# Optimization experiments

Hardware: AMD Instinct MI355X
Metric: run time of the kernel (lower is better)

Reference implementation:

```python
import jax, jax.numpy as jnp
import numpy as np

N = 100000   # nodes per branch
E = 1600000  # edges per branch
B = 512      # graphs in batch
D = 256      # input feature dim
C = 27       # number of side-effect labels
NEG_SLOPE = 0.2


def _gat_conv(x, src, dst, W, a_src, a_dst, b):
    """PyG GATConv, heads=1, with self loops. x:[N,din], src/dst:[E+N]."""
    n = x.shape[0]
    h = x @ W                               # [N, dout]
    al_s = h @ a_src                        # [N]
    al_d = h @ a_dst                        # [N]
    e = jax.nn.leaky_relu(al_s[src] + al_d[dst], NEG_SLOPE)  # [E+N]
    # segment softmax over destination nodes (self loops guarantee non-empty)
    m = jax.ops.segment_max(e, dst, num_segments=n)
    w = jnp.exp(e - m[dst])
    denom = jax.ops.segment_sum(w, dst, num_segments=n)
    alpha = w / denom[dst]                  # [E+N]
    out = jax.ops.segment_sum(h[src] * alpha[:, None], dst, num_segments=n)
    return out + b


def _with_self_loops(edge_index, n):
    loop = jnp.arange(n, dtype=edge_index.dtype)
    src = jnp.concatenate([edge_index[0], loop])
    dst = jnp.concatenate([edge_index[1], loop])
    return src, dst


def _mean_pool(x, batch, num_graphs):
    s = jax.ops.segment_sum(x, batch, num_segments=num_graphs)
    cnt = jax.ops.segment_sum(jnp.ones(x.shape[0], x.dtype), batch, num_segments=num_graphs)
    return s / jnp.maximum(cnt, 1.0)[:, None]


def _gat_params(key, din, dout):
    k = jax.random.split(key, 4)
    sc = 1.0 / np.sqrt(din)
    return (jax.random.normal(k[0], (din, dout), jnp.float32) * sc,
            jax.random.normal(k[1], (dout,), jnp.float32) * sc,
            jax.random.normal(k[2], (dout,), jnp.float32) * sc,
            jnp.zeros((dout,), jnp.float32))


def setup_inputs() -> dict:
    key = jax.random.key(0)
    ks = jax.random.split(key, 12)
    inp = {
        'x_s': jax.random.normal(ks[0], (N, D), jnp.float32),
        'x_t': jax.random.normal(ks[1], (N, D), jnp.float32),
        'edge_index_s': jax.random.randint(ks[2], (2, E), 0, N, jnp.int32),
        'edge_index_t': jax.random.randint(ks[3], (2, E), 0, N, jnp.int32),
        'xs_batch': jnp.sort(jax.random.randint(ks[4], (N,), 0, B, jnp.int32)),
        'xt_batch': jnp.sort(jax.random.randint(ks[5], (N,), 0, B, jnp.int32)),
    }
    for name, kk, din, dout in [('s1', ks[6], D, D // 2), ('s2', ks[7], D // 2, D // 4),
                                 ('t1', ks[8], D, D // 2), ('t2', ks[9], D // 2, D // 4)]:
        W, a_s, a_d, b = _gat_params(kk, din, dout)
        inp[f'W_{name}'] = W
        inp[f'a_src_{name}'] = a_s
        inp[f'a_dst_{name}'] = a_d
        inp[f'b_{name}'] = b
    inp['lin_w'] = jax.random.normal(ks[10], (D // 4, C), jnp.float32) / np.sqrt(D // 4)
    inp['lin_b'] = jnp.zeros((C,), jnp.float32)
    return inp


def reference(x_s, x_t,
              W_s1, a_src_s1, a_dst_s1, b_s1,
              W_s2, a_src_s2, a_dst_s2, b_s2,
              W_t1, a_src_t1, a_dst_t1, b_t1,
              W_t2, a_src_t2, a_dst_t2, b_t2,
              lin_w, lin_b,
              edge_index_s, edge_index_t, xs_batch, xt_batch):
    src_s, dst_s = _with_self_loops(edge_index_s, N)
    src_t, dst_t = _with_self_loops(edge_index_t, N)

    x1 = _gat_conv(x_s, src_s, dst_s, W_s1, a_src_s1, a_dst_s1, b_s1)
    x2 = _gat_conv(x1, src_s, dst_s, W_s2, a_src_s2, a_dst_s2, b_s2)
    xs = _mean_pool(x2, xs_batch, B)

    x3 = _gat_conv(x_t, src_t, dst_t, W_t1, a_src_t1, a_dst_t1, b_t1)
    x4 = _gat_conv(x3, src_t, dst_t, W_t2, a_src_t2, a_dst_t2, b_t2)
    xt = _mean_pool(x4, xt_batch, B)

    out = (xs + xt) @ lin_w + lin_b        # [B, C]
    return jax.nn.sigmoid(out)
```

## Files before the change

kernel.cpp:

```cpp
#include <hip/hip_runtime.h>
#include <hip/hip_bf16.h>
#include <math.h>

#define NEG_SLOPE 0.2f

static const int NN = 100000;
static const int EE = 1600000;
static const int BB = 512;
static const int NTOT = 2 * NN;
static const int ETOT = 2 * EE;
static const int NBUK = (NTOT + 511) / 512;
static const int CHUNK = 4096;
static const int NBLK = (ETOT + CHUNK - 1) / CHUNK;
static const int GB = (NN + 63) / 64;

typedef __attribute__((ext_vector_type(8))) short bf16x8;
typedef __attribute__((ext_vector_type(4))) float f32x4;

__device__ __forceinline__ float leaky(float x) { return x >= 0.f ? x : NEG_SLOPE * x; }

__device__ __forceinline__ unsigned short f2b(float f) {
    __hip_bfloat16 h = __float2bfloat16(f);
    return *reinterpret_cast<unsigned short*>(&h);
}
__device__ __forceinline__ float b2f_lo(unsigned v) { return __uint_as_float(v << 16); }
__device__ __forceinline__ float b2f_hi(unsigned v) { return __uint_as_float(v & 0xFFFF0000u); }
__device__ __forceinline__ unsigned packb(float a, float b) {
    return (unsigned)f2b(a) | ((unsigned)f2b(b) << 16);
}

__global__ void wt2_kernel(const float* __restrict__ Ws, const float* __restrict__ Wt_,
                           unsigned short* __restrict__ WT, int K, int N) {
    int idx = blockIdx.x * blockDim.x + threadIdx.x;
    if (idx >= 2 * K * N) return;
    int br = idx >= K * N;
    int j = idx - br * K * N;
    int n = j / K, k = j - n * K;
    const float* W = br ? Wt_ : Ws;
    WT[idx] = f2b(W[(size_t)k * N + n]);
}

template <int K, int N, bool ABF>
__global__ __launch_bounds__(256, 3) void gemm_fused_kernel(
        const void* __restrict__ Av_s, const void* __restrict__ Av_t,
        const unsigned short* __restrict__ WT,
        const float* __restrict__ as_s, const float* __restrict__ ad_s,
        const float* __restrict__ as_t, const float* __restrict__ ad_t,
        unsigned* __restrict__ hb, float* __restrict__ al_s, float* __restrict__ al_d,
        int nblk) {
    constexpr int NT2 = N / 32;
    __shared__ float als0[64], ald0[64];
    const int bid = blockIdx.x;
    const int br = (bid >= nblk) ? 1 : 0;
    const int lb = bid - br * nblk;
    const int t = threadIdx.x;
    const int l = t & 63, w = t >> 6;
    const int wm = w >> 1, wn = w & 1;
    const int rl = l & 15, kh = l >> 4;
    const int row0 = lb * 64 + wm * 32;
    const int r0 = min(row0 + rl, NN - 1);
    const int r1 = min(row0 + 16 + rl, NN - 1);
    const void* Av = br ? Av_t : Av_s;
    const unsigned short* WTb = WT + (size_t)br * N * K;
    const float* asv = br ? as_t : as_s;
    const float* adv = br ? ad_t : ad_s;

    f32x4 acc[2][NT2];
    #pragma unroll
    for (int g = 0; g < 2; g++)
        #pragma unroll
        for (int q = 0; q < NT2; q++) acc[g][q] = (f32x4){0.f, 0.f, 0.f, 0.f};

    if constexpr (ABF) {
        const unsigned short* A = (const unsigned short*)Av;
        bf16x8 A0[4], A1[4];
        #pragma unroll
        for (int kb = 0; kb < 4; kb++) {
            A0[kb] = *(const bf16x8*)(A + (size_t)r0 * K + kb * 32 + kh * 8);
            A1[kb] = *(const bf16x8*)(A + (size_t)r1 * K + kb * 32 + kh * 8);
        }
        #pragma unroll
        for (int kb = 0; kb < 4; kb++) {
            #pragma unroll
            for (int q = 0; q < NT2; q++) {
                int c = wn * (N / 2) + q * 16 + rl;
                bf16x8 bv = *(const bf16x8*)(WTb + (size_t)c * K + kb * 32 + kh * 8);
                acc[0][q] = __builtin_amdgcn_mfma_f32_16x16x32_bf16(A0[kb], bv, acc[0][q], 0, 0, 0);
                acc[1][q] = __builtin_amdgcn_mfma_f32_16x16x32_bf16(A1[kb], bv, acc[1][q], 0, 0, 0);
            }
        }
    } else {
        const float* A = (const float*)Av;
        #pragma unroll
        for (int kc = 0; kc < K; kc += 128) {
            float4 A0[8], A1[8];
            #pragma unroll
            for (int kb = 0; kb < 4; kb++) {
                const float* p0 = A + (size_t)r0 * K + kc + kb * 32 + kh * 8;
                const float* p1 = A + (size_t)r1 * K + kc + kb * 32 + kh * 8;
                A0[2 * kb] = *(const float4*)p0;
                A0[2 * kb + 1] = *(const float4*)(p0 + 4);
                A1[2 * kb] = *(const float4*)p1;
                A1[2 * kb + 1] = *(const float4*)(p1 + 4);
            }
            #pragma unroll
            for (int kb = 0; kb < 4; kb++) {
                float4 x0 = A0[2 * kb], x1 = A0[2 * kb + 1];
                float4 y0 = A1[2 * kb], y1 = A1[2 * kb + 1];
                union { bf16x8 v; unsigned short u[8]; } au, bu;
                au.u[0] = f2b(x0.x); au.u[1] = f2b(x0.y); au.u[2] = f2b(x0.z); au.u[3] = f2b(x0.w);
                au.u[4] = f2b(x1.x); au.u[5] = f2b(x1.y); au.u[6] = f2b(x1.z); au.u[7] = f2b(x1.w);
                bu.u[0] = f2b(y0.x); bu.u[1] = f2b(y0.y); bu.u[2] = f2b(y0.z); bu.u[3] = f2b(y0.w);
                bu.u[4] = f2b(y1.x); bu.u[5] = f2b(y1.y); bu.u[6] = f2b(y1.z); bu.u[7] = f2b(y1.w);
                #pragma unroll
                for (int q = 0; q < NT2; q++) {
                    int c = wn * (N / 2) + q * 16 + rl;
                    bf16x8 bv = *(const bf16x8*)(WTb + (size_t)c * K + kc + kb * 32 + kh * 8);
                    acc[0][q] = __builtin_amdgcn_mfma_f32_16x16x32_bf16(au.v, bv, acc[0][q], 0, 0, 0);
                    acc[1][q] = __builtin_amdgcn_mfma_f32_16x16x32_bf16(bu.v, bv, acc[1][q], 0, 0, 0);
                }
            }
        }
    }

    float asr[NT2], adr[NT2];
    #pragma unroll
    for (int q = 0; q < NT2; q++) {
        int c = wn * (N / 2) + q * 16 + rl;
        asr[q] = asv[c];
        adr[q] = adv[c];
    }

    float psA[2][4], pdA[2][4];
    #pragma unroll
    for (int rg = 0; rg < 2; rg++) {
        #pragma unroll
        for (int i = 0; i < 4; i++) {
            float ps = 0.f, pd = 0.f;
            #pragma unroll
            for (int q = 0; q < NT2; q++) {
                float v = acc[rg][q][i];
                ps += v * asr[q];
                pd += v * adr[q];
            }
            #pragma unroll
            for (int off = 1; off < 16; off <<= 1) {
                ps += __shfl_xor(ps, off);
                pd += __shfl_xor(pd, off);
            }
            psA[rg][i] = ps;
            pdA[rg][i] = pd;
        }
    }
    if (wn == 0 && rl == 0) {
        #pragma unroll
        for (int rg = 0; rg < 2; rg++)
            #pragma unroll
            for (int i = 0; i < 4; i++) {
                int rloc = wm * 32 + rg * 16 + kh * 4 + i;
                als0[rloc] = psA[rg][i];
                ald0[rloc] = pdA[rg][i];
            }
    }
    __syncthreads();
    if (wn == 1 && rl == 0) {
        #pragma unroll
        for (int rg = 0; rg < 2; rg++)
            #pragma unroll
            for (int i = 0; i < 4; i++) {
                int rloc = wm * 32 + rg * 16 + kh * 4 + i;
                int rlocal = lb * 64 + rloc;
                if (rlocal < NN) {
                    int g = br * NN + rlocal;
                    al_s[g] = psA[rg][i] + als0[rloc];
                    al_d[g] = pdA[rg][i] + ald0[rloc];
                }
            }
    }
    #pragma unroll
    for (int rg = 0; rg < 2; rg++) {
        #pragma unroll
        for (int i = 0; i < 4; i++) {
            int rlocal = lb * 64 + wm * 32 + rg * 16 + kh * 4 + i;
            bool ok = (rlocal < NN);
            int g = br * NN + rlocal;
            #pragma unroll
            for (int q = 0; q < NT2; q++) {
                float v = acc[rg][q][i];
                float hi = __shfl_xor(v, 1);
                if (ok && !(rl & 1)) {
                    int c = wn * (N / 2) + q * 16 + rl;
                    hb[(size_t)g * (N / 2) + (c >> 1)] = packb(v, hi);
                }
            }
        }
    }
}

__global__ __launch_bounds__(256) void bin_sort_kernel(const int* __restrict__ src_s,
                                                       const int* __restrict__ dst_s,
                                                       const int* __restrict__ src_t,
                                                       const int* __restrict__ dst_t,
                                                       uint2* __restrict__ region,
                                                       int* __restrict__ shist) {
    __shared__ int hist[512];
    __shared__ int part[256];
    __shared__ int cur[512];
    __shared__ uint2 lbuf[CHUNK];
    const int b = blockIdx.x, t = threadIdx.x;
    const int base = b * CHUNK;
    const int cnt = min(CHUNK, ETOT - base);
    hist[t] = 0; hist[t + 256] = 0;
    __syncthreads();
    unsigned es[16], ed[16];
    #pragma unroll
    for (int i = 0; i < 16; i++) {
        int li = i * 256 + t;
        if (li < cnt) {
            int e = base + li;
            if (e < EE) {
                es[i] = (unsigned)src_s[e];
                ed[i] = (unsigned)dst_s[e];
            } else {
                es[i] = (unsigned)src_t[e - EE] + NN;
                ed[i] = (unsigned)dst_t[e - EE] + NN;
            }
            atomicAdd(&hist[ed[i] >> 9], 1);
        }
    }
    __syncthreads();
    int d0 = hist[2 * t], d1 = hist[2 * t + 1];
    int s = d0 + d1;
    part[t] = s;
    __syncthreads();
    for (int off = 1; off < 256; off <<= 1) {
        int u = (t >= off) ? part[t - off] : 0;
        __syncthreads();
        part[t] += u;
        __syncthreads();
    }
    int ex = part[t] - s;
    cur[2 * t] = ex;
    cur[2 * t + 1] = ex + d0;
    if (2 * t < NBUK + 1) shist[(2 * t) * NBLK + b] = ex;
    if (2 * t + 1 < NBUK + 1) shist[(2 * t + 1) * NBLK + b] = ex + d0;
    __syncthreads();
    #pragma unroll
    for (int i = 0; i < 16; i++) {
        int li = i * 256 + t;
        if (li < cnt) {
            int slot = atomicAdd(&cur[ed[i] >> 9], 1);
            lbuf[slot] = make_uint2(es[i], ed[i]);
        }
    }
    __syncthreads();
    for (int i = t; i < cnt; i += 256) region[base + i] = lbuf[i];
}

__global__ void bucket_tot_kernel(const int* __restrict__ shist, int* __restrict__ btot) {
    __shared__ int red[256];
    const int k = blockIdx.x, t = threadIdx.x;
    int s = 0;
    for (int b = t; b < NBLK; b += 256)
        s += shist[(k + 1) * NBLK + b] - shist[k * NBLK + b];
    red[t] = s;
    __syncthreads();
    for (int off = 128; off > 0; off >>= 1) {
        if (t < off) red[t] += red[t + off];
        __syncthreads();
    }
    if (t == 0) btot[k] = red[0];
}

__global__ void bucket_scan_kernel(const int* __restrict__ btot, int* __restrict__ bbase) {
    __shared__ int part[256];
    int t = threadIdx.x;
    int v0 = (2 * t < NBUK) ? btot[2 * t] : 0;
    int v1 = (2 * t + 1 < NBUK) ? btot[2 * t + 1] : 0;
    int s = v0 + v1;
    part[t] = s;
    __syncthreads();
    for (int off = 1; off < 256; off <<= 1) {
        int u = (t >= off) ? part[t - off] : 0;
        __syncthreads();
        part[t] += u;
        __syncthreads();
    }
    int ex = part[t] - s;
    if (2 * t < NBUK) bbase[2 * t] = ex;
    if (2 * t + 1 < NBUK) bbase[2 * t + 1] = ex + v0;
}

__global__ __launch_bounds__(256) void csr_bucket_kernel(const uint2* __restrict__ region,
                                                         const int* __restrict__ shist,
                                                         const int* __restrict__ bbase,
                                                         int* __restrict__ rowptr,
                                                         int* __restrict__ col) {
    __shared__ int deg[512];
    __shared__ int part[256];
    __shared__ int cur[512];
    const int k = blockIdx.x, t = threadIdx.x;
    const int n0 = k * 512;
    const int nloc = min(512, NTOT - n0);
    const int base = bbase[k];
    deg[t] = 0; deg[t + 256] = 0;
    __syncthreads();
    for (int b = t; b < NBLK; b += 256) {
        int s0 = shist[k * NBLK + b], s1 = shist[(k + 1) * NBLK + b];
        for (int i = s0; i < s1; i++) {
            uint2 e = region[(size_t)b * CHUNK + i];
            atomicAdd(&deg[(int)e.y - n0], 1);
        }
    }
    __syncthreads();
    int d0 = deg[2 * t], d1 = deg[2 * t + 1];
    int s = d0 + d1;
    part[t] = s;
    __syncthreads();
    for (int off = 1; off < 256; off <<= 1) {
        int u = (t >= off) ? part[t - off] : 0;
        __syncthreads();
        part[t] += u;
        __syncthreads();
    }
    int ex = part[t] - s;
    cur[2 * t] = ex;
    cur[2 * t + 1] = ex + d0;
    if (2 * t < nloc) rowptr[n0 + 2 * t] = base + ex;
    if (2 * t + 1 < nloc) rowptr[n0 + 2 * t + 1] = base + ex + d0;
    if (t == 0 && n0 + nloc == NTOT) rowptr[NTOT] = base + part[255];
    __syncthreads();
    for (int b = t; b < NBLK; b += 256) {
        int s0 = shist[k * NBLK + b], s1 = shist[(k + 1) * NBLK + b];
        for (int i = s0; i < s1; i++) {
            uint2 e = region[(size_t)b * CHUNK + i];
            int pos = atomicAdd(&cur[(int)e.y - n0], 1);
            col[base + pos] = (int)e.x;
        }
    }
}

__global__ void brow2_kernel(const int* __restrict__ bs, const int* __restrict__ bt,
                             int* __restrict__ brow_s, int* __restrict__ brow_t) {
    int g = blockIdx.x * blockDim.x + threadIdx.x;
    const int* batch;
    int* brow;
    int gg;
    if (g <= BB) { batch = bs; brow = brow_s; gg = g; }
    else if (g <= 2 * BB + 1) { batch = bt; brow = brow_t; gg = g - (BB + 1); }
    else return;
    int lo = 0, hi = NN;
    while (lo < hi) {
        int mid = (lo + hi) >> 1;
        if (batch[mid] < gg) lo = mid + 1; else hi = mid;
    }
    brow[gg] = lo;
}

__global__ void gat_gather128_kernel(const int* __restrict__ rowptr, const int* __restrict__ col,
                                     const float* __restrict__ al_s, const float* __restrict__ al_d,
                                     const unsigned* __restrict__ hb,
                                     const float* __restrict__ bias_s,
                                     const float* __restrict__ bias_t,
                                     unsigned* __restrict__ outb) {
    int node = blockIdx.x * 4 + (threadIdx.x >> 6);
    int lane = threadIdx.x & 63;
    if (node >= NTOT) return;
    const float* bias = (node < NN) ? bias_s : bias_t;
    const int slot = lane >> 4, sub = lane & 15;
    const int beg = rowptr[node], end = rowptr[node + 1];
    const float ald = al_d[node];
    const float e_self = leaky(al_s[node] + ald);

    float acc[8] = {};
    float dsum = 0.f;
    for (int base = beg; base < end; base += 64) {
        int i = base + lane;
        float w = 0.f; int s = 0;
        if (i < end) {
            s = col[i];
            w = expf(leaky(al_s[s] + ald));
        }
        dsum += w;
        int cnt = min(64, end - base);
        for (int j = 0; j < cnt; j += 4) {
            int idx = j + slot;
            float wj = __shfl(w, idx);
            int sj = __shfl(s, idx);
            uint4 v = *(const uint4*)(hb + (size_t)sj * 64 + sub * 4);
            acc[0] += wj * b2f_lo(v.x); acc[1] += wj * b2f_hi(v.x);
            acc[2] += wj * b2f_lo(v.y); acc[3] += wj * b2f_hi(v.y);
            acc[4] += wj * b2f_lo(v.z); acc[5] += wj * b2f_hi(v.z);
            acc[6] += wj * b2f_lo(v.w); acc[7] += wj * b2f_hi(v.w);
        }
    }
    #pragma unroll
    for (int k = 0; k < 8; k++) {
        acc[k] += __shfl_xor(acc[k], 16);
        acc[k] += __shfl_xor(acc[k], 32);
    }
    #pragma unroll
    for (int off = 32; off > 0; off >>= 1) dsum += __shfl_xor(dsum, off);

    float wself = expf(e_self);
    dsum += wself;
    float inv = 1.f / dsum;
    if (slot == 0) {
        uint4 sv = *(const uint4*)(hb + (size_t)node * 64 + sub * 4);
        float sf[8] = { b2f_lo(sv.x), b2f_hi(sv.x), b2f_lo(sv.y), b2f_hi(sv.y),
                        b2f_lo(sv.z), b2f_hi(sv.z), b2f_lo(sv.w), b2f_hi(sv.w) };
        float o[8];
        #pragma unroll
        for (int k = 0; k < 8; k++)
            o[k] = bias[sub * 8 + k] + (acc[k] + wself * sf[k]) * inv;
        uint4 r = make_uint4(packb(o[0], o[1]), packb(o[2], o[3]),
                             packb(o[4], o[5]), packb(o[6], o[7]));
        *(uint4*)(outb + (size_t)node * 64 + sub * 4) = r;
    }
}

__global__ void gat_gather64_kernel(const int* __restrict__ rowptr, const int* __restrict__ col,
                                    const float* __restrict__ al_s, const float* __restrict__ al_d,
                                    const unsigned* __restrict__ hb,
                                    const float* __restrict__ bias_s,
                                    const float* __restrict__ bias_t,
                                    float* __restrict__ out) {
    int node = blockIdx.x * 4 + (threadIdx.x >> 6);
    int lane = threadIdx.x & 63;
    if (node >= NTOT) return;
    const float* bias = (node < NN) ? bias_s : bias_t;
    const int slot = lane >> 4, sub = lane & 15;
    const int beg = rowptr[node], end = rowptr[node + 1];
    const float ald = al_d[node];
    const float e_self = leaky(al_s[node] + ald);

    float acc[4] = {};
    float dsum = 0.f;
    for (int base = beg; base < end; base += 64) {
        int i = base + lane;
        float w = 0.f; int s = 0;
        if (i < end) {
            s = col[i];
            w = expf(leaky(al_s[s] + ald));
        }
        dsum += w;
        int cnt = min(64, end - base);
        for (int j = 0; j < cnt; j += 4) {
            int idx = j + slot;
            float wj = __shfl(w, idx);
            int sj = __shfl(s, idx);
            uint2 v = *(const uint2*)(hb + (size_t)sj * 32 + sub * 2);
            acc[0] += wj * b2f_lo(v.x); acc[1] += wj * b2f_hi(v.x);
            acc[2] += wj * b2f_lo(v.y); acc[3] += wj * b2f_hi(v.y);
        }
    }
    #pragma unroll
    for (int k = 0; k < 4; k++) {
        acc[k] += __shfl_xor(acc[k], 16);
        acc[k] += __shfl_xor(acc[k], 32);
    }
    #pragma unroll
    for (int off = 32; off > 0; off >>= 1) dsum += __shfl_xor(dsum, off);

    float wself = expf(e_self);
    dsum += wself;
    float inv = 1.f / dsum;
    if (slot == 0) {
        uint2 sv = *(const uint2*)(hb + (size_t)node * 32 + sub * 2);
        float sf[4] = { b2f_lo(sv.x), b2f_hi(sv.x), b2f_lo(sv.y), b2f_hi(sv.y) };
        float4 o;
        o.x = bias[sub * 4 + 0] + (acc[0] + wself * sf[0]) * inv;
        o.y = bias[sub * 4 + 1] + (acc[1] + wself * sf[1]) * inv;
        o.z = bias[sub * 4 + 2] + (acc[2] + wself * sf[2]) * inv;
        o.w = bias[sub * 4 + 3] + (acc[3] + wself * sf[3]) * inv;
        *(float4*)(out + (size_t)node * 64 + sub * 4) = o;
    }
}

__global__ void pool_seg_kernel(const float* __restrict__ x,
                                const int* __restrict__ brow_s, const int* __restrict__ brow_t,
                                float* __restrict__ pooled_s, float* __restrict__ pooled_t) {
    __shared__ float red[4][64];
    int g = blockIdx.x;
    int tb = g >= BB;
    int gb = g - tb * BB;
    const int* brow = tb ? brow_t : brow_s;
    float* pooled = tb ? pooled_t : pooled_s;
    int off = tb ? NN : 0;
    int lane = threadIdx.x & 63, w = threadIdx.x >> 6;
    int beg = brow[gb], end = brow[gb + 1];
    float acc = 0.f;
    for (int n = beg + w; n < end; n += 4)
        acc += x[(size_t)(off + n) * 64 + lane];
    red[w][lane] = acc;
    __syncthreads();
    if (w == 0) {
        float s = red[0][lane] + red[1][lane] + red[2][lane] + red[3][lane];
        float cnt = (float)(end - beg);
        pooled[(size_t)gb * 64 + lane] = s / fmaxf(cnt, 1.f);
    }
}

__global__ void final_kernel(const float* __restrict__ ps, const float* __restrict__ pt,
                             const float* __restrict__ lw, const float* __restrict__ lb,
                             float* __restrict__ out) {
    int g = blockIdx.x;
    int c = threadIdx.x;
    if (c >= 27) return;
    float acc = lb[c];
    #pragma unroll 8
    for (int k = 0; k < 64; k++) {
        float xv = ps[g * 64 + k] + pt[g * 64 + k];
        acc += xv * lw[k * 27 + c];
    }
    out[g * 27 + c] = 1.f / (1.f + expf(-acc));
}

extern "C" void kernel_launch(void* const* d_in, const int* in_sizes, int n_in,
                              void* d_out, int out_size, void* d_ws, size_t ws_size,
                              hipStream_t stream) {
    const float* x_s = (const float*)d_in[0];
    const float* x_t = (const float*)d_in[1];
    const int* ei_s = (const int*)d_in[2];
    const int* ei_t = (const int*)d_in[3];
    const int* xs_batch = (const int*)d_in[4];
    const int* xt_batch = (const int*)d_in[5];
    const float* W_s1 = (const float*)d_in[6];
    const float* a_src_s1 = (const float*)d_in[7];
    const float* a_dst_s1 = (const float*)d_in[8];
    const float* b_s1 = (const float*)d_in[9];
    const float* W_s2 = (const float*)d_in[10];
    const float* a_src_s2 = (const float*)d_in[11];
    const float* a_dst_s2 = (const float*)d_in[12];
    const float* b_s2 = (const float*)d_in[13];
    const float* W_t1 = (const float*)d_in[14];
    const float* a_src_t1 = (const float*)d_in[15];
    const float* a_dst_t1 = (const float*)d_in[16];
    const float* b_t1 = (const float*)d_in[17];
    const float* W_t2 = (const float*)d_in[18];
    const float* a_src_t2 = (const float*)d_in[19];
    const float* a_dst_t2 = (const float*)d_in[20];
    const float* b_t2 = (const float*)d_in[21];
    const float* lin_w = (const float*)d_in[22];
    const float* lin_b = (const float*)d_in[23];
    float* out = (float*)d_out;

    unsigned* hb = (unsigned*)d_ws;
    uint2* region = (uint2*)d_ws;
    unsigned* out1b = hb + (size_t)NTOT * 64;
    float* out2 = (float*)out1b;
    int* col = (int*)(out1b + (size_t)NTOT * 64);
    float* al_s = (float*)(col + ETOT);
    float* al_d = al_s + NTOT;
    float* pooled_s = al_d + NTOT;
    float* pooled_t = pooled_s + (size_t)BB * 64;
    unsigned short* WT1 = (unsigned short*)(pooled_t + (size_t)BB * 64);
    unsigned short* WT2 = WT1 + 2 * 256 * 128;
    int* rowptr = (int*)(WT2 + 2 * 128 * 64);
    int* shist = rowptr + NTOT + 1;
    int* btot = shist + (NBUK + 1) * NBLK;
    int* bbase = btot + NBUK;
    int* brow_s = bbase + NBUK;
    int* brow_t = brow_s + BB + 1;

    const int* src_s = ei_s;
    const int* dst_s = ei_s + EE;
    const int* src_t = ei_t;
    const int* dst_t = ei_t + EE;

    bin_sort_kernel<<<NBLK, 256, 0, stream>>>(src_s, dst_s, src_t, dst_t, region, shist);
    bucket_tot_kernel<<<NBUK, 256, 0, stream>>>(shist, btot);
    bucket_scan_kernel<<<1, 256, 0, stream>>>(btot, bbase);
    csr_bucket_kernel<<<NBUK, 256, 0, stream>>>(region, shist, bbase, rowptr, col);

    wt2_kernel<<<(2 * 256 * 128 + 255) / 256, 256, 0, stream>>>(W_s1, W_t1, WT1, 256, 128);
    gemm_fused_kernel<256, 128, false><<<2 * GB, 256, 0, stream>>>(
        x_s, x_t, WT1, a_src_s1, a_dst_s1, a_src_t1, a_dst_t1, hb, al_s, al_d, GB);
    gat_gather128_kernel<<<(NTOT + 3) / 4, 256, 0, stream>>>(
        rowptr, col, al_s, al_d, hb, b_s1, b_t1, out1b);

    wt2_kernel<<<(2 * 128 * 64 + 255) / 256, 256, 0, stream>>>(W_s2, W_t2, WT2, 128, 64);
    gemm_fused_kernel<128, 64, true><<<2 * GB, 256, 0, stream>>>(
        out1b, (const unsigned short*)out1b + (size_t)NN * 128, WT2,
        a_src_s2, a_dst_s2, a_src_t2, a_dst_t2, hb, al_s, al_d, GB);
    gat_gather64_kernel<<<(NTOT + 3) / 4, 256, 0, stream>>>(
        rowptr, col, al_s, al_d, hb, b_s2, b_t2, out2);

    brow2_kernel<<<(2 * (BB + 1) + 255) / 256, 256, 0, stream>>>(xs_batch, xt_batch, brow_s, brow_t);
    pool_seg_kernel<<<2 * BB, 256, 0, stream>>>(out2, brow_s, brow_t, pooled_s, pooled_t);
    final_kernel<<<BB, 32, 0, stream>>>(pooled_s, pooled_t, lin_w, lin_b, out);
}
```

Measured before the change: 518.1 us.

## Stage GEMM A tiles through LDS with swizzle; unroll edge gather loops by two

The fused GEMM now copies each 64-row A tile in two K-halves from global memory into shared memory using direct global-to-LDS loads with an XOR swizzle, then reads MFMA operands from LDS. Previously each lane loaded scattered row fragments straight from global memory. This is meant to make the A loads coalesced and to prefetch B fragments per half. Separately, both aggregation kernels now process two neighbors per iteration so more gathers are in flight. The edge loop can read past cnt within the 64-lane chunk, but those lanes carry w=0 and s=0, so it is still safe. The costs are extra LDS use and two barriers per half, which may reduce occupancy.

```diff
diff --git a/kernel.cpp b/kernel.cpp
--- a/kernel.cpp
+++ b/kernel.cpp
@@ -29,6 +29,12 @@
     return (unsigned)f2b(a) | ((unsigned)f2b(b) << 16);
 }
 
+__device__ __forceinline__ void gload_lds16(const void* g, void* l) {
+    __builtin_amdgcn_global_load_lds(
+        (const __attribute__((address_space(1))) void*)g,
+        (__attribute__((address_space(3))) void*)l, 16, 0, 0);
+}
+
 __global__ void wt2_kernel(const float* __restrict__ Ws, const float* __restrict__ Wt_,
                            unsigned short* __restrict__ WT, int K, int N) {
     int idx = blockIdx.x * blockDim.x + threadIdx.x;
@@ -49,7 +55,17 @@
         unsigned* __restrict__ hb, float* __restrict__ al_s, float* __restrict__ al_d,
         int nblk) {
     constexpr int NT2 = N / 32;
+    constexpr int ES = ABF ? 2 : 4;
+    constexpr int ROWB = (K / 2) * ES;
+    constexpr int CPR = ROWB / 16;
+    constexpr int STB = 64 * ROWB;
+    constexpr int IPW = (STB / 16) / 256;
+    constexpr int SWZ = (CPR - 1) < 15 ? (CPR - 1) : 15;
+    constexpr int KBH = (K / 2) / 32;
+
+    __shared__ __align__(16) unsigned char Atile[STB];
     __shared__ float als0[64], ald0[64];
+
     const int bid = blockIdx.x;
     const int br = (bid >= nblk) ? 1 : 0;
     const int lb = bid - br * nblk;
@@ -57,10 +73,8 @@
     const int l = t & 63, w = t >> 6;
     const int wm = w >> 1, wn = w & 1;
     const int rl = l & 15, kh = l >> 4;
-    const int row0 = lb * 64 + wm * 32;
-    const int r0 = min(row0 + rl, NN - 1);
-    const int r1 = min(row0 + 16 + rl, NN - 1);
-    const void* Av = br ? Av_t : Av_s;
+    const int row0blk = lb * 64;
+    const char* Ab = (const char*)(br ? Av_t : Av_s);
     const unsigned short* WTb = WT + (size_t)br * N * K;
     const float* asv = br ? as_t : as_s;
     const float* adv = br ? ad_t : ad_s;
@@ -71,56 +85,58 @@
         #pragma unroll
         for (int q = 0; q < NT2; q++) acc[g][q] = (f32x4){0.f, 0.f, 0.f, 0.f};
 
-    if constexpr (ABF) {
-        const unsigned short* A = (const unsigned short*)Av;
-        bf16x8 A0[4], A1[4];
-        #pragma unroll
-        for (int kb = 0; kb < 4; kb++) {
-            A0[kb] = *(const bf16x8*)(A + (size_t)r0 * K + kb * 32 + kh * 8);
-            A1[kb] = *(const bf16x8*)(A + (size_t)r1 * K + kb * 32 + kh * 8);
-        }
-        #pragma unroll
-        for (int kb = 0; kb < 4; kb++) {
+    #pragma unroll
+    for (int h = 0; h < 2; h++) {
+        #pragma unroll
+        for (int i = 0; i < IPW; i++) {
+            int c = (i * 4 + w) * 64 + l;
+            int row = c / CPR, jp = c % CPR;
+            int jg = jp ^ (row & SWZ);
+            int rowg = min(row0blk + row, NN - 1);
+            const char* src = Ab + ((size_t)rowg * K + h * (K / 2)) * ES + jg * 16;
+            gload_lds16(src, Atile + c * 16);
+        }
+        bf16x8 Bv[KBH * NT2];
+        #pragma unroll
+        for (int kb = 0; kb < KBH; kb++)
             #pragma unroll
             for (int q = 0; q < NT2; q++) {
                 int c = wn * (N / 2) + q * 16 + rl;
-                bf16x8 bv = *(const bf16x8*)(WTb + (size_t)c * K + kb * 32 + kh * 8);
-                acc[0][q] = __builtin_amdgcn_mfma_f32_16x16x32_bf16(A0[kb], bv, acc[0][q], 0, 0, 0);
-                acc[1][q] = __builtin_amdgcn_mfma_f32_16x16x32_bf16(A1[kb], bv, acc[1][q], 0, 0, 0);
-            }
-        }
-    } else {
-        const float* A = (const float*)Av;
-        #pragma unroll
-        for (int kc = 0; kc < K; kc += 128) {
-            float4 A0[8], A1[8];
-            #pragma unroll
-            for (int kb = 0; kb < 4; kb++) {
-                const float* p0 = A + (size_t)r0 * K + kc + kb * 32 + kh * 8;
-                const float* p1 = A + (size_t)r1 * K + kc + kb * 32 + kh * 8;
-                A0[2 * kb] = *(const float4*)p0;
-                A0[2 * kb + 1] = *(const float4*)(p0 + 4);
-                A1[2 * kb] = *(const float4*)p1;
-                A1[2 * kb + 1] = *(const float4*)(p1 + 4);
-            }
-            #pragma unroll
-            for (int kb = 0; kb < 4; kb++) {
-                float4 x0 = A0[2 * kb], x1 = A0[2 * kb + 1];
-                float4 y0 = A1[2 * kb], y1 = A1[2 * kb + 1];
-                union { bf16x8 v; unsigned short u[8]; } au, bu;
-                au.u[0] = f2b(x0.x); au.u[1] = f2b(x0.y); au.u[2] = f2b(x0.z); au.u[3] = f2b(x0.w);
-                au.u[4] = f2b(x1.x); au.u[5] = f2b(x1.y); au.u[6] = f2b(x1.z); au.u[7] = f2b(x1.w);
-                bu.u[0] = f2b(y0.x); bu.u[1] = f2b(y0.y); bu.u[2] = f2b(y0.z); bu.u[3] = f2b(y0.w);
-                bu.u[4] = f2b(y1.x); bu.u[5] = f2b(y1.y); bu.u[6] = f2b(y1.z); bu.u[7] = f2b(y1.w);
-                #pragma unroll
-                for (int q = 0; q < NT2; q++) {
-                    int c = wn * (N / 2) + q * 16 + rl;
-                    bf16x8 bv = *(const bf16x8*)(WTb + (size_t)c * K + kc + kb * 32 + kh * 8);
-                    acc[0][q] = __builtin_amdgcn_mfma_f32_16x16x32_bf16(au.v, bv, acc[0][q], 0, 0, 0);
-                    acc[1][q] = __builtin_amdgcn_mfma_f32_16x16x32_bf16(bu.v, bv, acc[1][q], 0, 0, 0);
+                Bv[kb * NT2 + q] =
+                    *(const bf16x8*)(WTb + (size_t)c * K + h * (K / 2) + kb * 32 + kh * 8);
+            }
+        __syncthreads();
+        #pragma unroll
+        for (int kb = 0; kb < KBH; kb++) {
+            bf16x8 av[2];
+            #pragma unroll
+            for (int rg = 0; rg < 2; rg++) {
+                int r = wm * 32 + rg * 16 + rl;
+                if constexpr (ABF) {
+                    int j = kb * 4 + kh;
+                    int js = j ^ (r & SWZ);
+                    av[rg] = *(const bf16x8*)(Atile + r * ROWB + js * 16);
+                } else {
+                    int j0 = kb * 8 + kh * 2;
+                    int j0s = j0 ^ (r & SWZ);
+                    int j1s = (j0 + 1) ^ (r & SWZ);
+                    float4 fa = *(const float4*)(Atile + r * ROWB + j0s * 16);
+                    float4 fb = *(const float4*)(Atile + r * ROWB + j1s * 16);
+                    union { bf16x8 v; unsigned short u[8]; } au;
+                    au.u[0] = f2b(fa.x); au.u[1] = f2b(fa.y);
+                    au.u[2] = f2b(fa.z); au.u[3] = f2b(fa.w);
+                    au.u[4] = f2b(fb.x); au.u[5] = f2b(fb.y);
+                    au.u[6] = f2b(fb.z); au.u[7] = f2b(fb.w);
+                    av[rg] = au.v;
                 }
             }
-        }
+            #pragma unroll
+            for (int q = 0; q < NT2; q++) {
+                acc[0][q] = __builtin_amdgcn_mfma_f32_16x16x32_bf16(av[0], Bv[kb * NT2 + q], acc[0][q], 0, 0, 0);
+                acc[1][q] = __builtin_amdgcn_mfma_f32_16x16x32_bf16(av[1], Bv[kb * NT2 + q], acc[1][q], 0, 0, 0);
+            }
+        }
+        __syncthreads();
     }
 
     float asr[NT2], adr[NT2];
@@ -383,15 +399,20 @@
         }
         dsum += w;
         int cnt = min(64, end - base);
-        for (int j = 0; j < cnt; j += 4) {
-            int idx = j + slot;
-            float wj = __shfl(w, idx);
-            int sj = __shfl(s, idx);
-            uint4 v = *(const uint4*)(hb + (size_t)sj * 64 + sub * 4);
-            acc[0] += wj * b2f_lo(v.x); acc[1] += wj * b2f_hi(v.x);
-            acc[2] += wj * b2f_lo(v.y); acc[3] += wj * b2f_hi(v.y);
-            acc[4] += wj * b2f_lo(v.z); acc[5] += wj * b2f_hi(v.z);
-            acc[6] += wj * b2f_lo(v.w); acc[7] += wj * b2f_hi(v.w);
+        for (int j = 0; j < cnt; j += 8) {
+            int idx0 = j + slot, idx1 = j + 4 + slot;
+            float w0 = __shfl(w, idx0), w1 = __shfl(w, idx1);
+            int s0 = __shfl(s, idx0), s1 = __shfl(s, idx1);
+            uint4 v0 = *(const uint4*)(hb + (size_t)s0 * 64 + sub * 4);
+            uint4 v1 = *(const uint4*)(hb + (size_t)s1 * 64 + sub * 4);
+            acc[0] += w0 * b2f_lo(v0.x); acc[1] += w0 * b2f_hi(v0.x);
+            acc[2] += w0 * b2f_lo(v0.y); acc[3] += w0 * b2f_hi(v0.y);
+            acc[4] += w0 * b2f_lo(v0.z); acc[5] += w0 * b2f_hi(v0.z);
+            acc[6] += w0 * b2f_lo(v0.w); acc[7] += w0 * b2f_hi(v0.w);
+            acc[0] += w1 * b2f_lo(v1.x); acc[1] += w1 * b2f_hi(v1.x);
+            acc[2] += w1 * b2f_lo(v1.y); acc[3] += w1 * b2f_hi(v1.y);
+            acc[4] += w1 * b2f_lo(v1.z); acc[5] += w1 * b2f_hi(v1.z);
+            acc[6] += w1 * b2f_lo(v1.w); acc[7] += w1 * b2f_hi(v1.w);
         }
     }
     #pragma unroll
@@ -445,13 +466,16 @@
         }
         dsum += w;
         int cnt = min(64, end - base);
-        for (int j = 0; j < cnt; j += 4) {
-            int idx = j + slot;
-            float wj = __shfl(w, idx);
-            int sj = __shfl(s, idx);
-            uint2 v = *(const uint2*)(hb + (size_t)sj * 32 + sub * 2);
-            acc[0] += wj * b2f_lo(v.x); acc[1] += wj * b2f_hi(v.x);
-            acc[2] += wj * b2f_lo(v.y); acc[3] += wj * b2f_hi(v.y);
+        for (int j = 0; j < cnt; j += 8) {
+            int idx0 = j + slot, idx1 = j + 4 + slot;
+            float w0 = __shfl(w, idx0), w1 = __shfl(w, idx1);
+            int s0 = __shfl(s, idx0), s1 = __shfl(s, idx1);
+            uint2 v0 = *(const uint2*)(hb + (size_t)s0 * 32 + sub * 2);
+            uint2 v1 = *(const uint2*)(hb + (size_t)s1 * 32 + sub * 2);
+            acc[0] += w0 * b2f_lo(v0.x); acc[1] += w0 * b2f_hi(v0.x);
+            acc[2] += w0 * b2f_lo(v0.y); acc[3] += w0 * b2f_hi(v0.y);
+            acc[0] += w1 * b2f_lo(v1.x); acc[1] += w1 * b2f_hi(v1.x);
+            acc[2] += w1 * b2f_lo(v1.y); acc[3] += w1 * b2f_hi(v1.y);
         }
     }
     #pragma unroll
```

Result: faster. 457.8 us (-11.6%).
